# Optimization experiments

Hardware: AMD Instinct MI355X
Metric: run time of the kernel (lower is better)

The kernel has to match this reference:

```python
import jax, jax.numpy as jnp
import numpy as np

B, S, D_IN, D_MODEL = 128, 2048, 512, 2048
M, NSY, H, T = 25, 64, 8, 10
REP = NSY * (NSY + 1) // 2
OUT_DIMS = S * 2
DH = D_IN // H
IU, JU = np.triu_indices(NSY)
IDX_OUT = np.arange(NSY)                      # 'first-last': first n neurons for out sync
IDX_ACT = np.arange(D_MODEL - NSY, D_MODEL)   # last n neurons for action sync


def _ln(x, g, b):
    mu = x.mean(-1, keepdims=True)
    var = x.var(-1, keepdims=True)
    return (x - mu) / jnp.sqrt(var + 1e-5) * g + b


def _sync(act, alpha, beta, r, idx):
    # pairwise upper-triangle outer product without materializing (B,n,n)
    sel = act[:, idx]
    pair = sel[:, IU] * sel[:, JU]  # (B, REP)
    if alpha is None:
        alpha, beta = pair, jnp.ones_like(pair)
    else:
        alpha = r * alpha + pair
        beta = r * beta + 1.0
    return alpha / jnp.sqrt(beta), alpha, beta


def _forward(tokens, emb, W_pos, b_pos, Wq, bq, Wk, bk, Wv, bv, Wo, bo, Ws, bs,
             ln_s_g, ln_s_b, ln_n_g, ln_n_b, Wn, bn, temp, Wout, bout,
             start_act, start_trace, decay_action, decay_out):
    # rotary-style learned positional embedding: rotate [0,1] by theta in [0,180deg]
    thetas = jnp.deg2rad(jnp.linspace(0.0, 180.0, S))
    rotated = jnp.stack([-jnp.sin(thetas), jnp.cos(thetas)], -1)  # (S,2)
    pe = rotated @ W_pos + b_pos                                   # (S, D_IN)
    feats = emb[tokens] + pe[None]                                 # (B,S,D_IN)
    kh = (feats @ Wk + bk).reshape(B, S, H, DH)
    vh = (feats @ Wv + bv).reshape(B, S, H, DH)
    r_a = jnp.exp(-decay_action)[None]
    r_o = jnp.exp(-decay_out)[None]
    act = jnp.broadcast_to(start_act[None], (B, D_MODEL))
    trace = jnp.broadcast_to(start_trace[None], (B, D_MODEL, M))
    a_a = b_a = a_o = b_o = None
    preds, certs = [], []
    for _ in range(T):
        s_act, a_a, b_a = _sync(act, a_a, b_a, r_a, IDX_ACT)
        q = (s_act @ Wq + bq).reshape(B, H, DH)
        scores = jnp.einsum('bhd,bshd->bhs', q, kh) / np.float32(np.sqrt(DH))
        attn = jax.nn.softmax(scores, -1)
        o = jnp.einsum('bhs,bshd->bhd', attn, vh).reshape(B, D_IN) @ Wo + bo
        # SynapseNet: Linear -> GLU -> LayerNorm
        pre = jnp.concatenate([o, act], -1) @ Ws + bs
        g1, g2 = jnp.split(pre, 2, -1)
        state = _ln(g1 * jax.nn.sigmoid(g2), ln_s_g, ln_s_b)  # (B, D_MODEL)
        trace = jnp.concatenate([trace[:, :, 1:], state[:, :, None]], -1)
        # NLM: per-neuron linear over memory, GLU, temperature
        xn = _ln(trace, ln_n_g, ln_n_b)
        y = jnp.einsum('bnm,mon->bno', xn, Wn) + bn  # (B, D_MODEL, 2)
        act = (y[..., 0] * jax.nn.sigmoid(y[..., 1])) / temp
        s_out, a_o, b_o = _sync(act, a_o, b_o, r_o, IDX_OUT)
        pred = s_out @ Wout + bout  # (B, OUT_DIMS)
        preds.append(pred)
        logits = pred.reshape(B, S, 2)
        p = jax.nn.softmax(logits, -1)
        ent = -(p * jax.nn.log_softmax(logits, -1)).sum(-1) / np.float32(np.log(2.0))
        ne = ent.mean(-1)
        certs.append(jnp.stack([ne, 1.0 - ne], -1))
    return jnp.stack(preds, -1), jnp.stack(certs, -1)  # (B,OUT_DIMS,T),(B,2,T)


def setup_inputs() -> dict:
    key = jax.random.key(0)
    ks = jax.random.split(key, 16)
    def n(k, shape, s=0.02):
        return (jax.random.normal(k, shape) * s).astype(jnp.float32)
    bound = 1.0 / np.sqrt(M + 2)
    return {
        'tokens': jax.random.randint(ks[0], (B, S), 0, 2, dtype=jnp.int32),
        'emb': n(ks[1], (2, D_IN), 1.0),
        'W_pos': n(ks[2], (2, D_IN)), 'b_pos': jnp.zeros((D_IN,)),
        'Wq': n(ks[3], (REP, D_IN)), 'bq': jnp.zeros((D_IN,)),
        'Wk': n(ks[4], (D_IN, D_IN)), 'bk': jnp.zeros((D_IN,)),
        'Wv': n(ks[5], (D_IN, D_IN)), 'bv': jnp.zeros((D_IN,)),
        'Wo': n(ks[6], (D_IN, D_IN)), 'bo': jnp.zeros((D_IN,)),
        'Ws': n(ks[7], (D_IN + D_MODEL, 2 * D_MODEL)), 'bs': jnp.zeros((2 * D_MODEL,)),
        'ln_s_g': jnp.ones((D_MODEL,)), 'ln_s_b': jnp.zeros((D_MODEL,)),
        'ln_n_g': jnp.ones((M,)), 'ln_n_b': jnp.zeros((M,)),
        'Wn': jax.random.uniform(ks[8], (M, 2, D_MODEL), minval=-bound, maxval=bound),
        'bn': jnp.zeros((1, D_MODEL, 2)),
        'temp': jnp.ones((1,)),
        'Wout': n(ks[9], (REP, OUT_DIMS)), 'bout': jnp.zeros((OUT_DIMS,)),
        'start_act': n(ks[10], (D_MODEL,), 1.0),
        'start_trace': n(ks[11], (D_MODEL, M), 1.0),
        'decay_action': jax.random.uniform(ks[12], (REP,), minval=0.0, maxval=1.0),
        'decay_out': jax.random.uniform(ks[13], (REP,), minval=0.0, maxval=1.0),
    }


def reference(tokens, emb, W_pos, b_pos, Wq, bq, Wk, bk, Wv, bv, Wo, bo, Ws, bs,
              ln_s_g, ln_s_b, ln_n_g, ln_n_b, Wn, bn, temp, Wout, bout,
              start_act, start_trace, decay_action, decay_out):
    return _forward(tokens, emb, W_pos, b_pos, Wq, bq, Wk, bk, Wv, bv, Wo, bo, Ws, bs,
                    ln_s_g, ln_s_b, ln_n_g, ln_n_b, Wn, bn, temp, Wout, bout,
                    start_act, start_trace, decay_action, decay_out)
```

## Files before the change

### kernel.cpp

```cpp
#include <hip/hip_runtime.h>
#include <hip/hip_bf16.h>
#include <math.h>

#define B_ 128
#define S_ 2048
#define D_IN_ 512
#define D_MODEL_ 2048
#define M_ 25
#define NSY_ 64
#define H_ 8
#define T_ 10
#define REP_ 2080
#define DH_ 64
#define PRED_N (B_ * 4096)

typedef unsigned short ushort_t;
typedef __bf16 bf16x8 __attribute__((ext_vector_type(8)));
typedef float f32x4 __attribute__((ext_vector_type(4)));
typedef unsigned short us8 __attribute__((ext_vector_type(8)));

__device__ __forceinline__ ushort_t f2bf(float f) {
    __hip_bfloat16 h = __float2bfloat16(f);
    return *(ushort_t*)&h;
}

__global__ __launch_bounds__(256) void gemm_bf16(
    const float* __restrict__ A, int lda,
    const ushort_t* __restrict__ Bt, int ldb,
    const float* __restrict__ bias,
    float* __restrict__ C, int ldc,
    int M, int N, int K, int kchunk)
{
    const int nb = blockIdx.x, mb = blockIdx.y, zb = blockIdx.z;
    const int k0 = zb * kchunk;
    const int k1 = min(K, k0 + kchunk);
    __shared__ ushort_t As[64][40];
    __shared__ ushort_t Bs[128][40];

    const int tid  = threadIdx.x;
    const int wave = tid >> 6;
    const int lane = tid & 63;
    const int quad = lane >> 4;
    const int mrow = lane & 15;

    f32x4 acc[4][2];
    #pragma unroll
    for (int s = 0; s < 4; s++)
        #pragma unroll
        for (int u = 0; u < 2; u++)
            acc[s][u] = (f32x4){0.f, 0.f, 0.f, 0.f};

    const int arow = tid >> 2, akc = (tid & 3) * 8;
// ... 28 lines not shown
            for (int u = 0; u < 2; u++)
                acc[s][u] = __builtin_amdgcn_mfma_f32_16x16x32_bf16(
                    af[s], bfr[u], acc[s][u], 0, 0, 0);
        __syncthreads();
    }

    if (gridDim.z == 1) {
        #pragma unroll
        for (int s = 0; s < 4; s++)
            #pragma unroll
            for (int u = 0; u < 2; u++) {
                const int col = nb * 128 + wave * 32 + u * 16 + mrow;
                #pragma unroll
                for (int reg = 0; reg < 4; reg++) {
                    const int row = mb * 64 + s * 16 + quad * 4 + reg;
                    C[(size_t)row * ldc + col] = acc[s][u][reg] + bias[col];
                }
            }
    } else {
        #pragma unroll
        for (int s = 0; s < 4; s++)
            #pragma unroll
            for (int u = 0; u < 2; u++) {
                const int col = nb * 128 + wave * 32 + u * 16 + mrow;
                #pragma unroll
                for (int reg = 0; reg < 4; reg++) {
                    const int row = mb * 64 + s * 16 + quad * 4 + reg;
                    atomicAdd(&C[(size_t)row * ldc + col], acc[s][u][reg]);
                }
            }
    }
}

__global__ __launch_bounds__(256) void gemm_bb(
    const ushort_t* __restrict__ A, int lda,
    const ushort_t* __restrict__ Bt, int ldb,
    const float* __restrict__ bias,
    float* __restrict__ C, int ldc,
    int M, int N, int K, int kchunk)
{
    const int nb = blockIdx.x, mb = blockIdx.y, zb = blockIdx.z;
    const int k0 = zb * kchunk;
    const int k1 = min(K, k0 + kchunk);
    __shared__ ushort_t As[64][40];
    __shared__ ushort_t Bs[128][40];

    const int tid  = threadIdx.x;
    const int wave = tid >> 6;
    const int lane = tid & 63;
    const int quad = lane >> 4;
    const int mrow = lane & 15;

    f32x4 acc[4][2];
    #pragma unroll
    for (int s = 0; s < 4; s++)
        #pragma unroll
        for (int u = 0; u < 2; u++)
            acc[s][u] = (f32x4){0.f, 0.f, 0.f, 0.f};

    const int arow = tid >> 2, akc = (tid & 3) * 8;
    const int brow = tid >> 1, bkc = (tid & 1) * 16;

    for (int kk0 = k0; kk0 < k1; kk0 += 32) {
        {
            const ushort_t* ap = A + (size_t)(mb * 64 + arow) * lda + kk0 + akc;
            *(us8*)&As[arow][akc] = *(const us8*)ap;
        }
        {
            const ushort_t* bp = Bt + (size_t)(nb * 128 + brow) * ldb + kk0 + bkc;
            *(us8*)&Bs[brow][bkc]     = *(const us8*)bp;
            *(us8*)&Bs[brow][bkc + 8] = *(const us8*)(bp + 8);
        }
        __syncthreads();

        bf16x8 af[4], bfr[2];
        #pragma unroll
        for (int s = 0; s < 4; s++)
            af[s] = *(const bf16x8*)&As[s * 16 + mrow][quad * 8];
        #pragma unroll
        for (int u = 0; u < 2; u++)
            bfr[u] = *(const bf16x8*)&Bs[wave * 32 + u * 16 + mrow][quad * 8];
        #pragma unroll
        for (int s = 0; s < 4; s++)
            #pragma unroll
            for (int u = 0; u < 2; u++)
                acc[s][u] = __builtin_amdgcn_mfma_f32_16x16x32_bf16(
                    af[s], bfr[u], acc[s][u], 0, 0, 0);
        __syncthreads();
    }

    if (gridDim.z == 1) {
        #pragma unroll
        for (int s = 0; s < 4; s++)
            #pragma unroll
            for (int u = 0; u < 2; u++) {
                const int col = nb * 128 + wave * 32 + u * 16 + mrow;
                #pragma unroll
                for (int reg = 0; reg < 4; reg++) {
                    const int row = mb * 64 + s * 16 + quad * 4 + reg;
                    C[(size_t)row * ldc + col] = acc[s][u][reg] + bias[col];
                }
            }
    } else {
        #pragma unroll
        for (int s = 0; s < 4; s++)
            #pragma unroll
            for (int u = 0; u < 2; u++) {
                const int col = nb * 128 + wave * 32 + u * 16 + mrow;
                #pragma unroll
                for (int reg = 0; reg < 4; reg++) {
                    const int row = mb * 64 + s * 16 + quad * 4 + reg;
                    atomicAdd(&C[(size_t)row * ldc + col], acc[s][u][reg]);
                }
            }
    }
}

__device__ __forceinline__ void g_tile128(
    const ushort_t* Ap, int lda, const ushort_t* Bt, int ldb,
    float* C, int ldc, int nb, int mb, int k0, int k1, char* smem, int tid)
{
    ushort_t (*As)[40] = (ushort_t(*)[40])smem;
    ushort_t (*Bs)[40] = (ushort_t(*)[40])(smem + 64 * 40 * 2);
    const int wave = tid >> 6;
    const int lane = tid & 63;
    const int quad = lane >> 4;
    const int mrow = lane & 15;

    f32x4 acc[4][2];
    #pragma unroll
    for (int s = 0; s < 4; s++)
        #pragma unroll
        for (int u = 0; u < 2; u++)
            acc[s][u] = (f32x4){0.f, 0.f, 0.f, 0.f};

    const int arow = tid >> 2, akc = (tid & 3) * 8;
    const int brow = tid >> 1, bkc = (tid & 1) * 16;

    for (int kk0 = k0; kk0 < k1; kk0 += 32) {
        {
            const ushort_t* ap = Ap + (size_t)(mb * 64 + arow) * lda + kk0 + akc;
            *(us8*)&As[arow][akc] = *(const us8*)ap;
        }
        {
            const ushort_t* bp = Bt + (size_t)(nb * 128 + brow) * ldb + kk0 + bkc;
            *(us8*)&Bs[brow][bkc]     = *(const us8*)bp;
            *(us8*)&Bs[brow][bkc + 8] = *(const us8*)(bp + 8);
        }
// ... 28 lines not shown
        }
}

__global__ __launch_bounds__(256) void triple_kernel(
    const ushort_t* __restrict__ s_outb, const ushort_t* __restrict__ WoutT,
    float* __restrict__ predt,
    const ushort_t* __restrict__ s_actb, const ushort_t* __restrict__ WqT,
    float* __restrict__ qbuf,
    const ushort_t* __restrict__ actb, const ushort_t* __restrict__ WsT,
    float* __restrict__ pre_nxt)
{
    __shared__ __align__(16) char smem[15360];
    const int vb = blockIdx.x, tid = threadIdx.x;
    if (vb < 320) {
        const int nb = vb & 31, mb = (vb >> 5) & 1, zb = vb >> 6;
        const int k0 = zb * 416;
        g_tile128(s_outb, REP_, WoutT, REP_, predt, 4096,
                  nb, mb, k0, min(REP_, k0 + 416), smem, tid);
    } else if (vb < 424) {
        const int v2 = vb - 320;
        const int nb = v2 & 3, mb = (v2 >> 2) & 1, zb = v2 >> 3;
        const int k0 = zb * 160;
        g_tile128(s_actb, REP_, WqT, REP_, qbuf, 512,
                  nb, mb, k0, min(REP_, k0 + 160), smem, tid);
    } else {
        const int v3 = vb - 424;
        const int nb = v3 & 31, mb = (v3 >> 5) & 1, zb = v3 >> 6;
        const int k0 = zb * 256;
        g_tile128(actb, 2048, WsT + 512, 2560, pre_nxt, 4096,
                  nb, mb, k0, k0 + 256, smem, tid);
    }
}

__global__ __launch_bounds__(256) void gemm_qk(
    const float* __restrict__ q,
    const ushort_t* __restrict__ Kb,
    float* __restrict__ sc)
{
    const int nb = blockIdx.x, mb = blockIdx.y, z = blockIdx.z;
    const int c = z >> 3, h = z & 7;
    __shared__ ushort_t As[64][40];
    __shared__ ushort_t Bs[128][40];

    const int tid  = threadIdx.x;
    const int wave = tid >> 6;
    const int lane = tid & 63;
    const int quad = lane >> 4;
    const int mrow = lane & 15;

    f32x4 acc[4][2];
    #pragma unroll
    for (int s = 0; s < 4; s++)
        #pragma unroll
        for (int u = 0; u < 2; u++)
            acc[s][u] = (f32x4){0.f, 0.f, 0.f, 0.f};

    const int arow = tid >> 2, akc = (tid & 3) * 8;
    const int brow = tid >> 1, bkc = (tid & 1) * 16;
    const float* Abase = q + (size_t)h * 64;
    const ushort_t* Bbase = Kb + (size_t)c * S_ * 512 + h * 64;

    #pragma unroll
    for (int kk0 = 0; kk0 < 64; kk0 += 32) {
        {
            const float* ap = Abase + (size_t)(mb * 64 + arow) * 512 + kk0 + akc;
            float4 v0 = *(const float4*)ap;
            float4 v1 = *(const float4*)(ap + 4);
            us8 w = { f2bf(v0.x), f2bf(v0.y), f2bf(v0.z), f2bf(v0.w),
                      f2bf(v1.x), f2bf(v1.y), f2bf(v1.z), f2bf(v1.w) };
            *(us8*)&As[arow][akc] = w;
        }
        {
            const ushort_t* bp = Bbase + (size_t)(nb * 128 + brow) * 512 + kk0 + bkc;
            *(us8*)&Bs[brow][bkc]     = *(const us8*)bp;
            *(us8*)&Bs[brow][bkc + 8] = *(const us8*)(bp + 8);
        }
        __syncthreads();

        bf16x8 af[4], bfr[2];
        #pragma unroll
        for (int s = 0; s < 4; s++)
            af[s] = *(const bf16x8*)&As[s * 16 + mrow][quad * 8];
        #pragma unroll
        for (int u = 0; u < 2; u++)
            bfr[u] = *(const bf16x8*)&Bs[wave * 32 + u * 16 + mrow][quad * 8];
        #pragma unroll
        for (int s = 0; s < 4; s++)
            #pragma unroll
            for (int u = 0; u < 2; u++)
                acc[s][u] = __builtin_amdgcn_mfma_f32_16x16x32_bf16(
                    af[s], bfr[u], acc[s][u], 0, 0, 0);
        __syncthreads();
    }

    float* Cb = sc + (size_t)z * 128 * S_;
    #pragma unroll
    for (int s = 0; s < 4; s++)
        #pragma unroll
        for (int u = 0; u < 2; u++) {
            const int col = nb * 128 + wave * 32 + u * 16 + mrow;
            #pragma unroll
            for (int reg = 0; reg < 4; reg++) {
                const int row = mb * 64 + s * 16 + quad * 4 + reg;
                Cb[(size_t)row * S_ + col] = 0.125f * acc[s][u][reg];
            }
        }
}

__global__ __launch_bounds__(256) void attn_soft(
    const float* __restrict__ sc,
    const int*   __restrict__ tokens,
    ushort_t* __restrict__ P,
    float* __restrict__ o,
    const float* __restrict__ bs2,
    float* __restrict__ pre_nxt)
{
    const int bh = blockIdx.x;
    const int b = bh >> 3, h = bh & 7;
    __shared__ float red[256];
    const int tid = threadIdx.x;

    if (bh < 512) {
        const int idx = bh * 256 + tid;
        const float4* bs4 = (const float4*)bs2;
        ((float4*)pre_nxt)[idx] = bs4[idx & 1023];
    } else if (bh < 576) {
        const int idx = (bh - 512) * 256 + tid;
        ((float4*)o)[idx] = make_float4(0.f, 0.f, 0.f, 0.f);
    }

    const float* sc0 = sc + ((size_t)h * 128 + b) * S_;
    const float* sc1 = sc + ((size_t)(8 + h) * 128 + b) * S_;
    const int* trow = tokens + (size_t)b * S_;

    int tok[8]; float sel[8];
    float lmax = -1e30f;
    #pragma unroll
    for (int i = 0; i < 8; i++) {
        const int s = tid + i * 256;
        tok[i] = trow[s];
        sel[i] = tok[i] ? sc1[s] : sc0[s];
        lmax = fmaxf(lmax, sel[i]);
    }
    red[tid] = lmax; __syncthreads();
    for (int off = 128; off > 0; off >>= 1) {
        if (tid < off) red[tid] = fmaxf(red[tid], red[tid + off]);
        __syncthreads();
    }
    const float mx = red[0];
    __syncthreads();

    float e[8];
    float lsum = 0.f;
    #pragma unroll
    for (int i = 0; i < 8; i++) {
        e[i] = expf(sel[i] - mx);
        lsum += e[i];
    }
    red[tid] = lsum; __syncthreads();
    for (int off = 128; off > 0; off >>= 1) {
        if (tid < off) red[tid] += red[tid + off];
        __syncthreads();
    }
    const float inv = 1.f / red[0];

    ushort_t* Pb = P + ((size_t)h * 128 + b) * 4096;
    #pragma unroll
    for (int i = 0; i < 8; i++) {
        const int s = tid + i * 256;
        const unsigned p = (unsigned)f2bf(e[i] * inv);
        const unsigned word = tok[i] ? (p << 16) : p;
        *(unsigned*)&Pb[s * 2] = word;
    }
}

__global__ __launch_bounds__(256) void gemm_pv(
    const ushort_t* __restrict__ P,
    const ushort_t* __restrict__ VT,
    float* __restrict__ o)
{
    const int mb = blockIdx.x, h = blockIdx.y, zb = blockIdx.z;
    const int k0 = zb * 512;
    __shared__ ushort_t As[64][40];
    __shared__ ushort_t Bs[64][40];

    const int tid  = threadIdx.x;
    const int wave = tid >> 6;
    const int lane = tid & 63;
    const int quad = lane >> 4;
    const int mrow = lane & 15;

    f32x4 acc[4];
    #pragma unroll
    for (int s = 0; s < 4; s++) acc[s] = (f32x4){0.f, 0.f, 0.f, 0.f};

    const int row = tid >> 2, kc = (tid & 3) * 8;
    const ushort_t* Ab = P  + ((size_t)h * 128 + mb * 64 + row) * 4096;
    const ushort_t* Bb = VT + ((size_t)h * 64 + row) * 4096;

    for (int kk = k0; kk < k0 + 512; kk += 32) {
        *(us8*)&As[row][kc] = *(const us8*)(Ab + kk + kc);
        *(us8*)&Bs[row][kc] = *(const us8*)(Bb + kk + kc);
        __syncthreads();
        bf16x8 bfr = *(const bf16x8*)&Bs[wave * 16 + mrow][quad * 8];
        #pragma unroll
        for (int s = 0; s < 4; s++) {
            bf16x8 af = *(const bf16x8*)&As[s * 16 + mrow][quad * 8];
            acc[s] = __builtin_amdgcn_mfma_f32_16x16x32_bf16(af, bfr, acc[s], 0, 0, 0);
        }
        __syncthreads();
    }

    const int col = h * 64 + wave * 16 + mrow;
    #pragma unroll
    for (int s = 0; s < 4; s++)
        #pragma unroll
        for (int reg = 0; reg < 4; reg++) {
            const int rowi = mb * 64 + s * 16 + quad * 4 + reg;
            atomicAdd(&o[(size_t)rowi * 512 + col], acc[s][reg]);
        }
}

__global__ void build_vt(const float* __restrict__ Vtab, ushort_t* __restrict__ VT)
{
    const int gid = blockIdx.x * 256 + threadIdx.x;
    const int k = gid & 4095;
    const int d = (gid >> 12) & 63;
    const int h = gid >> 18;
    const int s = k >> 1, c = k & 1;
    VT[gid] = f2bf(Vtab[((size_t)(c * S_ + s)) * 512 + h * 64 + d]);
}

#define IA_FE 8192
#define IA_AC (IA_FE + 1024)
#define IA_TR (IA_AC + 6400)
#define IA_SY (IA_TR + 9)
#define IA_NB (IA_SY + 1)
__global__ void init_all(const float* __restrict__ emb, const float* __restrict__ Wp,
                         const float* __restrict__ bp, float* __restrict__ f2,
                         const float* __restrict__ sa, float* __restrict__ act,
                         ushort_t* __restrict__ actb,
                         const float* __restrict__ st, float* __restrict__ trace,
                         const float* __restrict__ dec_act, const float* __restrict__ dec_out,
                         int* __restrict__ ijtab, float* __restrict__ r_act,
                         float* __restrict__ r_out, float* __restrict__ sqb_a,
                         float* __restrict__ sqb_o, float* __restrict__ zerov)
{
    const int vb = blockIdx.x, tid = threadIdx.x;
    if (vb < IA_FE) {
        const int gid = vb * 256 + tid;
        const int k = gid & 511;
        const int s = (gid >> 9) & (S_ - 1);
        const int c = gid >> 20;
        const float th = 3.14159265358979323846f * (float)s / (float)(S_ - 1);
        f2[gid] = emb[c * 512 + k] + (-sinf(th)) * Wp[k] + cosf(th) * Wp[512 + k] + bp[k];
    } else if (vb < IA_AC) {
        const int gid = (vb - IA_FE) * 256 + tid;
        const int n = gid & 2047;
        const float v = sa[n];
        act[gid] = v;
        actb[gid] = f2bf(v);
    } else if (vb < IA_TR) {
        const int idx4 = (vb - IA_AC) * 256 + tid;
        ((float4*)trace)[idx4] = ((const float4*)st)[idx4 % 12800];
    } else if (vb < IA_SY) {
        const int p = (vb - IA_TR) * 256 + tid;
        if (p >= REP_) return;
        int i = 0, rem = p;
        while (rem >= NSY_ - i) { rem -= NSY_ - i; i++; }
        ijtab[p] = (i << 16) | (i + rem);
        const float ra = expf(-dec_act[p]);
        const float ro = expf(-dec_out[p]);
        r_act[p] = ra; r_out[p] = ro;
        float ba = 1.f, bo2 = 1.f;
        sqb_a[p] = 1.f;
        sqb_o[p] = 1.f;
        for (int t = 1; t < T_; t++) {
            ba  = ra * ba  + 1.f;
            bo2 = ro * bo2 + 1.f;
            sqb_a[(size_t)t * REP_ + p] = sqrtf(ba);
            sqb_o[(size_t)t * REP_ + p] = sqrtf(bo2);
        }
    } else {
        #pragma unroll
        for (int k = 0; k < 4; k++)
            ((float4*)zerov)[tid * 4 + k] = make_float4(0.f, 0.f, 0.f, 0.f);
    }
}

__global__ __launch_bounds__(256) void transpose_all(
    const float* __restrict__ Wk, ushort_t* __restrict__ WkT,
    const float* __restrict__ Wv, ushort_t* __restrict__ WvT,
    const float* __restrict__ Wq, ushort_t* __restrict__ WqT,
    const float* __restrict__ Wo, ushort_t* __restrict__ WoT,
    const float* __restrict__ Ws, ushort_t* __restrict__ WsT,
    const float* __restrict__ Wout, ushort_t* __restrict__ WoutT)
{
    int bid = blockIdx.x;
    const float* in; ushort_t* out; int K, N;
    if      (bid <   256) {              in = Wk;   out = WkT;   K = 512;  N = 512;  }
    else if (bid <   512) { bid -=  256; in = Wv;   out = WvT;   K = 512;  N = 512;  }
    else if (bid <  1552) { bid -=  512; in = Wq;   out = WqT;   K = 2080; N = 512;  }
    else if (bid <  1808) { bid -= 1552; in = Wo;   out = WoT;   K = 512;  N = 512;  }
    else if (bid < 12048) { bid -= 1808; in = Ws;   out = WsT;   K = 2560; N = 4096; }
    else                  { bid -= 12048; in = Wout; out = WoutT; K = 2080; N = 4096; }
    const int bxw = N >> 5;
    const int bx = bid % bxw, by = bid / bxw;
    __shared__ float tile[32][33];
    const int k0 = by * 32, n0 = bx * 32;
    const int tx = threadIdx.x & 31, ty4 = (threadIdx.x >> 5) * 4;
    #pragma unroll
    for (int i = 0; i < 4; i++)
        tile[ty4 + i][tx] = in[(size_t)(k0 + ty4 + i) * N + n0 + tx];
    __syncthreads();
    #pragma unroll
    for (int i = 0; i < 4; i++)
        out[(size_t)(n0 + ty4 + i) * K + k0 + tx] = f2bf(tile[tx][ty4 + i]);
}

__global__ void cast_bf16_kernel(const float* __restrict__ src,
                                 __hip_bfloat16* __restrict__ dst, int n)
{
    const int gid = (blockIdx.x * 256 + threadIdx.x) * 4;
    if (gid >= n) return;
    float4 v = *(const float4*)(src + gid);
    dst[gid + 0] = __float2bfloat16(v.x);
    dst[gid + 1] = __float2bfloat16(v.y);
    dst[gid + 2] = __float2bfloat16(v.z);
    dst[gid + 3] = __float2bfloat16(v.w);
}

__global__ void bs2_kernel(const float* __restrict__ bs, const float* __restrict__ bo,
                           const float* __restrict__ Ws, float* __restrict__ bs2)
{
    const int n = blockIdx.x * 256 + threadIdx.x;
    float acc = bs[n];
    for (int j = 0; j < 512; j++)
        acc += bo[j] * Ws[(size_t)j * 4096 + n];
    bs2[n] = acc;
}

__global__ void sync_kernel(const float* __restrict__ act,
                            float* __restrict__ alpha,
                            const float* __restrict__ decay,
                            const int t, const int off,
                            ushort_t* __restrict__ sout,
                            float* __restrict__ ib1, const float* __restrict__ bias1, int iN1,
                            float* __restrict__ ib2, const float* __restrict__ bias2, int iN2)
{
    const int b = blockIdx.x;
    const int tid = threadIdx.x;
    if (blockIdx.y == 8) {
        if (ib1)
            for (int n = tid; n < iN1; n += 256)
                ib1[(size_t)b * iN1 + n] = bias1[n];
        if (ib2)
            for (int n = tid; n < iN2; n += 256)
                ib2[(size_t)b * iN2 + n] = bias2[n];
    }
    const int p = blockIdx.y * 256 + tid;
    if (p >= REP_) return;
    int i = 0, rem = p;
    while (rem >= NSY_ - i) { rem -= NSY_ - i; i++; }
    const int j = i + rem;
    const float si = act[(size_t)b * D_MODEL_ + off + i];
    const float sj = act[(size_t)b * D_MODEL_ + off + j];
    const float pair = si * sj;
    const float r = expf(-decay[p]);
    float a;
    if (t == 0) a = pair;
    else        a = r * alpha[(size_t)b * REP_ + p] + pair;
    alpha[(size_t)b * REP_ + p] = a;
// ... 89 lines not shown
        }
    }
    __syncthreads();

    if (half == 0) {
        for (int p = tid; p < REP_; p += 512) {
            const int ij = ijtab[p];
            const float pair = sh_sync[ij >> 16] * sh_sync[ij & 0xffff];
            const float r = r_out[p];
            float a2;
            if (TT == 0) a2 = pair;
            else         a2 = r * a_o[(size_t)b * REP_ + p] + pair;
            a_o[(size_t)b * REP_ + p] = a2;
            s_outb[(size_t)b * REP_ + p] = f2bf(a2 / sqb_out[(size_t)TT * REP_ + p]);
        }
        const float4* b4 = (const float4*)bout;
        float4* pd = (float4*)(predt + (size_t)b * 4096);
        for (int idx = tid; idx < 1024; idx += 512) pd[idx] = b4[idx];
    } else if (TT < T_ - 1) {
        for (int p = tid; p < REP_; p += 512) {
            const int ij = ijtab[p];
            const float pair = sh_sync[ij >> 16] * sh_sync[ij & 0xffff];
            const float r = r_act[p];
            float a2 = r * a_a[(size_t)b * REP_ + p] + pair;
            a_a[(size_t)b * REP_ + p] = a2;
            s_actb[(size_t)b * REP_ + p] = f2bf(a2 / sqb_act[(size_t)(TT + 1) * REP_ + p]);
        }
        const float4* b4 = (const float4*)bq;
        float4* qb = (float4*)(qbuf + (size_t)b * 512);
        if (tid < 128) qb[tid] = b4[tid];
    }
}

__global__ __launch_bounds__(256) void ent_all_kernel(
    const float* __restrict__ predst,
    float* __restrict__ certbf)
{
    const int t = blockIdx.x >> 7;
    const int b = blockIdx.x & 127;
    const int tid = threadIdx.x;
    __shared__ float red[256];
    const float* pr = predst + (size_t)t * PRED_N + (size_t)b * 4096;
    float sum = 0.f;
    #pragma unroll
    for (int i = 0; i < 8; i++) {
        const int s = tid + i * 256;
        const float l0 = pr[2 * s], l1 = pr[2 * s + 1];
        const float mm = fmaxf(l0, l1);
        const float z0 = expf(l0 - mm), z1 = expf(l1 - mm);
        const float Z = z0 + z1;
        const float lz = logf(Z);
        const float p0 = z0 / Z, p1 = z1 / Z;
        const float lp0 = (l0 - mm) - lz, lp1 = (l1 - mm) - lz;
        sum += -(p0 * lp0 + p1 * lp1) * 1.4426950408889634f;
    }
    red[tid] = sum; __syncthreads();
    for (int off = 128; off > 0; off >>= 1) {
        if (tid < off) red[tid] += red[tid + off];
        __syncthreads();
    }
    if (tid == 0) {
        const float ne = red[0] * (1.f / S_);
        certbf[(size_t)t * B_ * 2 + b * 2 + 0] = ne;
        certbf[(size_t)t * B_ * 2 + b * 2 + 1] = 1.f - ne;
    }
}

__global__ __launch_bounds__(256) void finalize_kernel(
    const float* __restrict__ predstage,
    const float* __restrict__ certbuf,
    float* __restrict__ dout)
{
    __shared__ float tile[T_][1024];
    const int tid = threadIdx.x;
    const int row0 = blockIdx.x * 1024;
    #pragma unroll
    for (int t = 0; t < T_; t++) {
        float4 v = *(const float4*)(predstage + (size_t)t * PRED_N + row0 + tid * 4);
        tile[t][tid * 4 + 0] = v.x; tile[t][tid * 4 + 1] = v.y;
        tile[t][tid * 4 + 2] = v.z; tile[t][tid * 4 + 3] = v.w;
    }
    __syncthreads();
    float buf[40];
    #pragma unroll
    for (int r = 0; r < 4; r++)
        #pragma unroll
        for (int t = 0; t < T_; t++)
            buf[r * 10 + t] = tile[t][tid * 4 + r];
    float* dst = dout + (size_t)(row0 + tid * 4) * T_;
    #pragma unroll
    for (int k = 0; k < 10; k++)
        *(float4*)(dst + k * 4) = make_float4(buf[4*k], buf[4*k+1], buf[4*k+2], buf[4*k+3]);

    if (blockIdx.x == 0 && tid < B_) {
        const int b = tid;
        const size_t base = (size_t)PRED_N * T_;
        #pragma unroll
        for (int t = 0; t < T_; t++) {
            dout[base + (size_t)(b * 2 + 0) * T_ + t] = certbuf[t * B_ * 2 + b * 2 + 0];
            dout[base + (size_t)(b * 2 + 1) * T_ + t] = certbuf[t * B_ * 2 + b * 2 + 1];
        }
    }
}

extern "C" void kernel_launch(void* const* d_in, const int* in_sizes, int n_in,
                              void* d_out, int out_size, void* d_ws, size_t ws_size,
                              hipStream_t stream)
{
    const int*   tokens    = (const int*)  d_in[0];
    const float* emb       = (const float*)d_in[1];
    const float* W_pos     = (const float*)d_in[2];
    const float* b_pos     = (const float*)d_in[3];
    const float* Wq        = (const float*)d_in[4];
    const float* bq        = (const float*)d_in[5];
    const float* Wk        = (const float*)d_in[6];
    const float* bk        = (const float*)d_in[7];
    const float* Wv        = (const float*)d_in[8];
    const float* bv        = (const float*)d_in[9];
    const float* Wo        = (const float*)d_in[10];
    const float* bo        = (const float*)d_in[11];
    const float* Ws        = (const float*)d_in[12];
    const float* bs        = (const float*)d_in[13];
    const float* ln_s_g    = (const float*)d_in[14];
    const float* ln_s_b    = (const float*)d_in[15];
    const float* ln_n_g    = (const float*)d_in[16];
    const float* ln_n_b    = (const float*)d_in[17];
    const float* Wn        = (const float*)d_in[18];
    const float* bn        = (const float*)d_in[19];
    const float* temp      = (const float*)d_in[20];
    const float* Wout      = (const float*)d_in[21];
    const float* bout      = (const float*)d_in[22];
    const float* start_act = (const float*)d_in[23];
    const float* start_tr  = (const float*)d_in[24];
    const float* dec_act   = (const float*)d_in[25];
    const float* dec_out   = (const float*)d_in[26];
    float* out = (float*)d_out;
    float* w = (float*)d_ws;

    size_t off = 0;
    float* f2     = w + off; off += (size_t)2 * S_ * 512;
    float* Ktab   = w + off; off += (size_t)2 * S_ * 512;
    float* Vtab   = w + off; off += (size_t)2 * S_ * 512;
    float* act    = w + off; off += (size_t)B_ * D_MODEL_;
    float* a_a    = w + off; off += (size_t)B_ * REP_;
    float* a_o    = w + off; off += (size_t)B_ * REP_;
    float* qbuf   = w + off; off += (size_t)B_ * 512;
    float* o_attn = w + off; off += (size_t)B_ * 512;
    float* pre0   = w + off; off += (size_t)B_ * 4096;
    float* pre1   = w + off; off += (size_t)B_ * 4096;
    float* trace  = w + off; off += (size_t)B_ * D_MODEL_ * M_;
    float* scbuf  = w + off; off += (size_t)16 * 128 * S_;
    float* predst = w + off; off += (size_t)T_ * PRED_N;
    float* certbf = w + off; off += (size_t)T_ * B_ * 2;
    float* Wcomb32= w + off; off += (size_t)4096 * 512;
    float* bs2    = w + off; off += 4096;
    float* zerov  = w + off; off += 4096;
    ushort_t* s_actb = (ushort_t*)(w + off); off += (size_t)B_ * REP_ / 2;
    ushort_t* s_outb = (ushort_t*)(w + off); off += (size_t)B_ * REP_ / 2;
    ushort_t* actb   = (ushort_t*)(w + off); off += (size_t)B_ * D_MODEL_ / 2;
    __hip_bfloat16* Kb = (__hip_bfloat16*)(w + off); off += (size_t)S_ * 512;
    ushort_t* Pbuf  = (ushort_t*)(w + off); off += (size_t)8 * 128 * 4096 / 2;
    ushort_t* VT    = (ushort_t*)(w + off); off += (size_t)8 * 64 * 4096 / 2;
    ushort_t* WkT   = (ushort_t*)(w + off); off += (size_t)512 * 512 / 2;
    ushort_t* WvT   = (ushort_t*)(w + off); off += (size_t)512 * 512 / 2;
    ushort_t* WqT   = (ushort_t*)(w + off); off += (size_t)512 * REP_ / 2;
    ushort_t* WoT   = (ushort_t*)(w + off); off += (size_t)512 * 512 / 2;
    ushort_t* WsT   = (ushort_t*)(w + off); off += (size_t)4096 * 2560 / 2;
    ushort_t* WoutT = (ushort_t*)(w + off); off += (size_t)4096 * REP_ / 2;
    ushort_t* WoC   = (ushort_t*)(w + off); off += (size_t)512 * 512 / 2;
    ushort_t* WcombTb=(ushort_t*)(w + off); off += (size_t)4096 * 512 / 2;
    int*   ijtab  = (int*)(w + off); off += REP_;
    float* r_actT = w + off; off += REP_;
    float* r_outT = w + off; off += REP_;
    float* sqb_a  = w + off; off += (size_t)T_ * REP_;
    float* sqb_o  = w + off; off += (size_t)T_ * REP_;

    init_all<<<IA_NB, 256, 0, stream>>>(
        emb, W_pos, b_pos, f2, start_act, act, actb, start_tr, trace,
        dec_act, dec_out, ijtab, r_actT, r_outT, sqb_a, sqb_o, zerov);
    transpose_all<<<20368, 256, 0, stream>>>(
        Wk, WkT, Wv, WvT, Wq, WqT, Wo, WoT, Ws, WsT, Wout, WoutT);
    gemm_bf16<<<dim3(4, 64, 1), 256, 0, stream>>>(
        f2, 512, WkT, 512, bk, Ktab, 512, 2 * S_, 512, 512, 512);
    gemm_bf16<<<dim3(4, 64, 1), 256, 0, stream>>>(
        f2, 512, WvT, 512, bv, Vtab, 512, 2 * S_, 512, 512, 512);
    cast_bf16_kernel<<<(2 * S_ * 512 / 4) / 256, 256, 0, stream>>>(Ktab, Kb, 2 * S_ * 512);
    build_vt<<<(8 * 64 * 4096) / 256, 256, 0, stream>>>(Vtab, VT);

    cast_bf16_kernel<<<(512 * 512 / 4) / 256, 256, 0, stream>>>(
        Wo, (__hip_bfloat16*)WoC, 512 * 512);
    gemm_bb<<<dim3(4, 64, 1), 256, 0, stream>>>(
        WsT, 2560, WoC, 512, zerov, Wcomb32, 512, 4096, 512, 512, 512);
    cast_bf16_kernel<<<(4096 * 512 / 4) / 256, 256, 0, stream>>>(
        Wcomb32, (__hip_bfloat16*)WcombTb, 4096 * 512);
    bs2_kernel<<<16, 256, 0, stream>>>(bs, bo, Ws, bs2);

    sync_kernel<<<dim3(B_, 9), 256, 0, stream>>>(
        act, a_a, dec_act, 0, D_MODEL_ - NSY_, s_actb,
        qbuf, bq, 512, pre0, bs2, 4096);
    gemm_bb<<<dim3(32, 2, 8), 256, 0, stream>>>(
        actb, 2048, WsT + 512, 2560, zerov, pre0, 4096, B_, 4096, 2048, 256);
    gemm_bb<<<dim3(4, 2, 13), 256, 0, stream>>>(
        s_actb, REP_, WqT, REP_, zerov, qbuf, 512, B_, 512, REP_, 160);

    #define ST_ARGS(PC, PT) \
        PC, ln_s_g, ln_s_b, trace, ln_n_g, ln_n_b, Wn, bn, temp, actb, \
        ijtab, r_outT, sqb_o, a_o, s_outb, bout, PT, \
        r_actT, sqb_a, a_a, s_actb, bq, qbuf

    for (int t = 0; t < T_; t++) {
        float* pre_cur = (t & 1) ? pre1 : pre0;
        float* pre_nxt = (t & 1) ? pre0 : pre1;
        float* predt = predst + (size_t)t * PRED_N;

        gemm_qk<<<dim3(S_ / 128, 2, 16), 256, 0, stream>>>(
            qbuf, (const ushort_t*)Kb, scbuf);
        attn_soft<<<B_ * H_, 256, 0, stream>>>(
            scbuf, tokens, Pbuf, o_attn, bs2, pre_nxt);
        gemm_pv<<<dim3(2, 8, 8), 256, 0, stream>>>(Pbuf, VT, o_attn);

        gemm_bf16<<<dim3(32, 2, 4), 256, 0, stream>>>(
            o_attn, 512, WcombTb, 512, bs2, pre_cur, 4096, B_, 4096, 512, 128);

        switch (t) {
            case 0: st_kernel<0><<<B_ * 2, 512, 0, stream>>>(ST_ARGS(pre_cur, predt)); break;
            case 1: st_kernel<1><<<B_ * 2, 512, 0, stream>>>(ST_ARGS(pre_cur, predt)); break;
            case 2: st_kernel<2><<<B_ * 2, 512, 0, stream>>>(ST_ARGS(pre_cur, predt)); break;
            case 3: st_kernel<3><<<B_ * 2, 512, 0, stream>>>(ST_ARGS(pre_cur, predt)); break;
            case 4: st_kernel<4><<<B_ * 2, 512, 0, stream>>>(ST_ARGS(pre_cur, predt)); break;
            case 5: st_kernel<5><<<B_ * 2, 512, 0, stream>>>(ST_ARGS(pre_cur, predt)); break;
            case 6: st_kernel<6><<<B_ * 2, 512, 0, stream>>>(ST_ARGS(pre_cur, predt)); break;
            case 7: st_kernel<7><<<B_ * 2, 512, 0, stream>>>(ST_ARGS(pre_cur, predt)); break;
            case 8: st_kernel<8><<<B_ * 2, 512, 0, stream>>>(ST_ARGS(pre_cur, predt)); break;
            case 9: st_kernel<9><<<B_ * 2, 512, 0, stream>>>(ST_ARGS(pre_cur, predt)); break;
        }

        const int nblk = (t < T_ - 1) ? 936 : 320;
        triple_kernel<<<nblk, 256, 0, stream>>>(
            s_outb, WoutT, predt, s_actb, WqT, qbuf, actb, WsT, pre_nxt);
    }

    ent_all_kernel<<<T_ * B_, 256, 0, stream>>>(predst, certbf);
    finalize_kernel<<<PRED_N / 1024, 256, 0, stream>>>(predst, certbf, out);
}
```

Measured before the change: 1.157 ms.

## Fuse setup kernels, select QK scores by token bitmask, merge epilogue kernels

Several setup launches are merged into a few multi-role kernels. The K/V projection GEMMs and the Wcomb GEMM become one grid, and the bf16 casts plus the V transpose become another. The initial Ws and Wq GEMMs are merged, and the Wo cast, bias fold and a token bitmask move into init_all. The QK kernel now writes only the score that matches each token's choice into a half-size buffer, which cuts score writes and the softmax read. The PV GEMM is split across more k-chunks, and the entropy and finalize kernels are fused into one per-batch epilogue. This trades fewer launches and less traffic for more divergent multi-role kernels and an epilogue grid of only 128 blocks.

```diff
diff --git a/kernel.cpp b/kernel.cpp
--- a/kernel.cpp
+++ b/kernel.cpp
@@ -18,6 +18,7 @@
 typedef __bf16 bf16x8 __attribute__((ext_vector_type(8)));
 typedef float f32x4 __attribute__((ext_vector_type(4)));
 typedef unsigned short us8 __attribute__((ext_vector_type(8)));
+typedef unsigned short us4 __attribute__((ext_vector_type(4)));
 
 __device__ __forceinline__ ushort_t f2bf(float f) {
     __hip_bfloat16 h = __float2bfloat16(f);
@@ -112,16 +113,18 @@
     }
 }
 
-__global__ __launch_bounds__(256) void gemm_bb(
-    const ushort_t* __restrict__ A, int lda,
-    const ushort_t* __restrict__ Bt, int ldb,
-    const float* __restrict__ bias,
-    float* __restrict__ C, int ldc,
-    int M, int N, int K, int kchunk)
-{
-    const int nb = blockIdx.x, mb = blockIdx.y, zb = blockIdx.z;
-    const int k0 = zb * kchunk;
-    const int k1 = min(K, k0 + kchunk);
+__global__ __launch_bounds__(256) void gemm3_kernel(
+    const float* __restrict__ f2,
+    const ushort_t* __restrict__ WkT, const float* __restrict__ bk, float* __restrict__ Ktab,
+    const ushort_t* __restrict__ WvT, const float* __restrict__ bv, float* __restrict__ Vtab,
+    const ushort_t* __restrict__ WsT, const ushort_t* __restrict__ WoC,
+    const float* __restrict__ zerov, float* __restrict__ Wcomb32)
+{
+    const int nb = blockIdx.x, mb = blockIdx.y, zs = blockIdx.z;
+    const ushort_t* Bt = (zs == 0) ? WkT : (zs == 1) ? WvT : WoC;
+    const float* bias  = (zs == 0) ? bk  : (zs == 1) ? bv  : zerov;
+    float* C           = (zs == 0) ? Ktab : (zs == 1) ? Vtab : Wcomb32;
+
     __shared__ ushort_t As[64][40];
     __shared__ ushort_t Bs[128][40];
 
@@ -141,13 +144,20 @@
     const int arow = tid >> 2, akc = (tid & 3) * 8;
     const int brow = tid >> 1, bkc = (tid & 1) * 16;
 
-    for (int kk0 = k0; kk0 < k1; kk0 += 32) {
+    for (int kk0 = 0; kk0 < 512; kk0 += 32) {
+        if (zs < 2) {
+            const float* ap = f2 + (size_t)(mb * 64 + arow) * 512 + kk0 + akc;
+            float4 v0 = *(const float4*)ap;
+            float4 v1 = *(const float4*)(ap + 4);
+            us8 w = { f2bf(v0.x), f2bf(v0.y), f2bf(v0.z), f2bf(v0.w),
+                      f2bf(v1.x), f2bf(v1.y), f2bf(v1.z), f2bf(v1.w) };
+            *(us8*)&As[arow][akc] = w;
+        } else {
+            const ushort_t* ap = WsT + (size_t)(mb * 64 + arow) * 2560 + kk0 + akc;
+            *(us8*)&As[arow][akc] = *(const us8*)ap;
+        }
         {
-            const ushort_t* ap = A + (size_t)(mb * 64 + arow) * lda + kk0 + akc;
-            *(us8*)&As[arow][akc] = *(const us8*)ap;
-        }
-        {
-            const ushort_t* bp = Bt + (size_t)(nb * 128 + brow) * ldb + kk0 + bkc;
+            const ushort_t* bp = Bt + (size_t)(nb * 128 + brow) * 512 + kk0 + bkc;
             *(us8*)&Bs[brow][bkc]     = *(const us8*)bp;
             *(us8*)&Bs[brow][bkc + 8] = *(const us8*)(bp + 8);
         }
@@ -169,31 +179,17 @@
         __syncthreads();
     }
 
-    if (gridDim.z == 1) {
-        #pragma unroll
-        for (int s = 0; s < 4; s++)
+    #pragma unroll
+    for (int s = 0; s < 4; s++)
+        #pragma unroll
+        for (int u = 0; u < 2; u++) {
+            const int col = nb * 128 + wave * 32 + u * 16 + mrow;
             #pragma unroll
-            for (int u = 0; u < 2; u++) {
-                const int col = nb * 128 + wave * 32 + u * 16 + mrow;
-                #pragma unroll
-                for (int reg = 0; reg < 4; reg++) {
-                    const int row = mb * 64 + s * 16 + quad * 4 + reg;
-                    C[(size_t)row * ldc + col] = acc[s][u][reg] + bias[col];
-                }
+            for (int reg = 0; reg < 4; reg++) {
+                const int row = mb * 64 + s * 16 + quad * 4 + reg;
+                C[(size_t)row * 512 + col] = acc[s][u][reg] + bias[col];
             }
-    } else {
-        #pragma unroll
-        for (int s = 0; s < 4; s++)
-            #pragma unroll
-            for (int u = 0; u < 2; u++) {
-                const int col = nb * 128 + wave * 32 + u * 16 + mrow;
-                #pragma unroll
-                for (int reg = 0; reg < 4; reg++) {
-                    const int row = mb * 64 + s * 16 + quad * 4 + reg;
-                    atomicAdd(&C[(size_t)row * ldc + col], acc[s][u][reg]);
-                }
-            }
-    }
+        }
 }
 
 __device__ __forceinline__ void g_tile128(
@@ -288,10 +284,33 @@
     }
 }
 
-__global__ __launch_bounds__(256) void gemm_qk(
+__global__ __launch_bounds__(256) void dual0_kernel(
+    const ushort_t* __restrict__ actb, const ushort_t* __restrict__ WsT,
+    float* __restrict__ pre0,
+    const ushort_t* __restrict__ s_actb, const ushort_t* __restrict__ WqT,
+    float* __restrict__ qbuf)
+{
+    __shared__ __align__(16) char smem[15360];
+    const int vb = blockIdx.x, tid = threadIdx.x;
+    if (vb < 512) {
+        const int nb = vb & 31, mb = (vb >> 5) & 1, zb = vb >> 6;
+        const int k0 = zb * 256;
+        g_tile128(actb, 2048, WsT + 512, 2560, pre0, 4096,
+                  nb, mb, k0, k0 + 256, smem, tid);
+    } else {
+        const int v2 = vb - 512;
+        const int nb = v2 & 3, mb = (v2 >> 2) & 1, zb = v2 >> 3;
+        const int k0 = zb * 160;
+        g_tile128(s_actb, REP_, WqT, REP_, qbuf, 512,
+                  nb, mb, k0, min(REP_, k0 + 160), smem, tid);
+    }
+}
+
+__global__ __launch_bounds__(256) void gemm_qk_sel(
     const float* __restrict__ q,
     const ushort_t* __restrict__ Kb,
-    float* __restrict__ sc)
+    const unsigned* __restrict__ tokbit,
+    float* __restrict__ scsel)
 {
     const int nb = blockIdx.x, mb = blockIdx.y, z = blockIdx.z;
     const int c = z >> 3, h = z & 7;
@@ -349,22 +368,34 @@
         __syncthreads();
     }
 
-    float* Cb = sc + (size_t)z * 128 * S_;
+    const int colw = nb * 4 + wave;
+    unsigned tb[16];
+    #pragma unroll
+    for (int s = 0; s < 4; s++)
+        #pragma unroll
+        for (int reg = 0; reg < 4; reg++) {
+            const int row = mb * 64 + s * 16 + quad * 4 + reg;
+            tb[s * 4 + reg] = tokbit[row * 64 + colw];
+        }
+
+    float* Cb = scsel + (size_t)h * 128 * S_;
     #pragma unroll
     for (int s = 0; s < 4; s++)
         #pragma unroll
         for (int u = 0; u < 2; u++) {
             const int col = nb * 128 + wave * 32 + u * 16 + mrow;
+            const int sh = (u * 16 + mrow) & 31;
             #pragma unroll
             for (int reg = 0; reg < 4; reg++) {
                 const int row = mb * 64 + s * 16 + quad * 4 + reg;
-                Cb[(size_t)row * S_ + col] = 0.125f * acc[s][u][reg];
+                if (((tb[s * 4 + reg] >> sh) & 1u) == (unsigned)c)
+                    Cb[(size_t)row * S_ + col] = 0.125f * acc[s][u][reg];
             }
         }
 }
 
 __global__ __launch_bounds__(256) void attn_soft(
-    const float* __restrict__ sc,
+    const float* __restrict__ scsel,
     const int*   __restrict__ tokens,
     ushort_t* __restrict__ P,
     float* __restrict__ o,
@@ -385,8 +416,7 @@
         ((float4*)o)[idx] = make_float4(0.f, 0.f, 0.f, 0.f);
     }
 
-    const float* sc0 = sc + ((size_t)h * 128 + b) * S_;
-    const float* sc1 = sc + ((size_t)(8 + h) * 128 + b) * S_;
+    const float* scs = scsel + ((size_t)h * 128 + b) * S_;
     const int* trow = tokens + (size_t)b * S_;
 
     int tok[8]; float sel[8];
@@ -395,7 +425,7 @@
     for (int i = 0; i < 8; i++) {
         const int s = tid + i * 256;
         tok[i] = trow[s];
-        sel[i] = tok[i] ? sc1[s] : sc0[s];
+        sel[i] = scs[s];
         lmax = fmaxf(lmax, sel[i]);
     }
     red[tid] = lmax; __syncthreads();
@@ -436,7 +466,7 @@
     float* __restrict__ o)
 {
     const int mb = blockIdx.x, h = blockIdx.y, zb = blockIdx.z;
-    const int k0 = zb * 512;
+    const int k0 = zb * 256;
     __shared__ ushort_t As[64][40];
     __shared__ ushort_t Bs[64][40];
 
@@ -454,7 +484,7 @@
     const ushort_t* Ab = P  + ((size_t)h * 128 + mb * 64 + row) * 4096;
     const ushort_t* Bb = VT + ((size_t)h * 64 + row) * 4096;
 
-    for (int kk = k0; kk < k0 + 512; kk += 32) {
+    for (int kk = k0; kk < k0 + 256; kk += 32) {
         *(us8*)&As[row][kc] = *(const us8*)(Ab + kk + kc);
         *(us8*)&Bs[row][kc] = *(const us8*)(Bb + kk + kc);
         __syncthreads();
@@ -475,23 +505,16 @@
             const int rowi = mb * 64 + s * 16 + quad * 4 + reg;
             atomicAdd(&o[(size_t)rowi * 512 + col], acc[s][reg]);
         }
-}
-
-__global__ void build_vt(const float* __restrict__ Vtab, ushort_t* __restrict__ VT)
-{
-    const int gid = blockIdx.x * 256 + threadIdx.x;
-    const int k = gid & 4095;
-    const int d = (gid >> 12) & 63;
-    const int h = gid >> 18;
-    const int s = k >> 1, c = k & 1;
-    VT[gid] = f2bf(Vtab[((size_t)(c * S_ + s)) * 512 + h * 64 + d]);
 }
 
 #define IA_FE 8192
 #define IA_AC (IA_FE + 1024)
 #define IA_TR (IA_AC + 6400)
 #define IA_SY (IA_TR + 9)
-#define IA_NB (IA_SY + 1)
+#define IA_ZV (IA_SY + 1)
+#define IA_WO (IA_ZV + 256)
+#define IA_BS (IA_WO + 16)
+#define IA_NB (IA_BS + 1024)
 __global__ void init_all(const float* __restrict__ emb, const float* __restrict__ Wp,
                          const float* __restrict__ bp, float* __restrict__ f2,
                          const float* __restrict__ sa, float* __restrict__ act,
@@ -500,7 +523,11 @@
                          const float* __restrict__ dec_act, const float* __restrict__ dec_out,
                          int* __restrict__ ijtab, float* __restrict__ r_act,
                          float* __restrict__ r_out, float* __restrict__ sqb_a,
-                         float* __restrict__ sqb_o, float* __restrict__ zerov)
+                         float* __restrict__ sqb_o, float* __restrict__ zerov,
+                         const float* __restrict__ Wo, ushort_t* __restrict__ WoC,
+                         const float* __restrict__ bs, const float* __restrict__ bo,
+                         const float* __restrict__ Ws, float* __restrict__ bs2,
+                         const int* __restrict__ tokens, unsigned* __restrict__ tokbit)
 {
     const int vb = blockIdx.x, tid = threadIdx.x;
     if (vb < IA_FE) {
@@ -537,10 +564,31 @@
             sqb_a[(size_t)t * REP_ + p] = sqrtf(ba);
             sqb_o[(size_t)t * REP_ + p] = sqrtf(bo2);
         }
-    } else {
+    } else if (vb < IA_ZV) {
         #pragma unroll
         for (int k = 0; k < 4; k++)
             ((float4*)zerov)[tid * 4 + k] = make_float4(0.f, 0.f, 0.f, 0.f);
+    } else if (vb < IA_WO) {
+        const int idx4 = (vb - IA_ZV) * 256 + tid;
+        float4 v = ((const float4*)Wo)[idx4];
+        us4 w = { f2bf(v.x), f2bf(v.y), f2bf(v.z), f2bf(v.w) };
+        ((us4*)WoC)[idx4] = w;
+    } else if (vb < IA_BS) {
+        const int n = (vb - IA_WO) * 256 + tid;
+        float acc = bs[n];
+        for (int j = 0; j < 512; j++)
+            acc += bo[j] * Ws[(size_t)j * 4096 + n];
+        bs2[n] = acc;
+    } else {
+        const int blk = vb - IA_BS;
+        const int b = blk >> 3, s0 = (blk & 7) * 256;
+        const int tok = tokens[(size_t)b * S_ + s0 + tid];
+        const unsigned long long m = __ballot(tok != 0);
+        if ((tid & 63) == 0) {
+            const int w = tid >> 6;
+            tokbit[b * 64 + (s0 >> 5) + w * 2]     = (unsigned)m;
+            tokbit[b * 64 + (s0 >> 5) + w * 2 + 1] = (unsigned)(m >> 32);
+        }
     }
 }
 
@@ -574,26 +622,29 @@
         out[(size_t)(n0 + ty4 + i) * K + k0 + tx] = f2bf(tile[tx][ty4 + i]);
 }
 
-__global__ void cast_bf16_kernel(const float* __restrict__ src,
-                                 __hip_bfloat16* __restrict__ dst, int n)
-{
-    const int gid = (blockIdx.x * 256 + threadIdx.x) * 4;
-    if (gid >= n) return;
-    float4 v = *(const float4*)(src + gid);
-    dst[gid + 0] = __float2bfloat16(v.x);
-    dst[gid + 1] = __float2bfloat16(v.y);
-    dst[gid + 2] = __float2bfloat16(v.z);
-    dst[gid + 3] = __float2bfloat16(v.w);
-}
-
-__global__ void bs2_kernel(const float* __restrict__ bs, const float* __restrict__ bo,
-                           const float* __restrict__ Ws, float* __restrict__ bs2)
-{
-    const int n = blockIdx.x * 256 + threadIdx.x;
-    float acc = bs[n];
-    for (int j = 0; j < 512; j++)
-        acc += bo[j] * Ws[(size_t)j * 4096 + n];
-    bs2[n] = acc;
+__global__ void cast3_kernel(const float* __restrict__ Ktab, ushort_t* __restrict__ Kb,
+                             const float* __restrict__ Vtab, ushort_t* __restrict__ VT,
+                             const float* __restrict__ Wcomb32, ushort_t* __restrict__ WcombTb)
+{
+    const int vb = blockIdx.x, tid = threadIdx.x;
+    if (vb < 2048) {
+        const int idx4 = vb * 256 + tid;
+        float4 v = ((const float4*)Ktab)[idx4];
+        us4 w = { f2bf(v.x), f2bf(v.y), f2bf(v.z), f2bf(v.w) };
+        ((us4*)Kb)[idx4] = w;
+    } else if (vb < 10240) {
+        const int gid = (vb - 2048) * 256 + tid;
+        const int k = gid & 4095;
+        const int d = (gid >> 12) & 63;
+        const int h = gid >> 18;
+        const int s = k >> 1, c = k & 1;
+        VT[gid] = f2bf(Vtab[((size_t)(c * S_ + s)) * 512 + h * 64 + d]);
+    } else {
+        const int idx4 = (vb - 10240) * 256 + tid;
+        float4 v = ((const float4*)Wcomb32)[idx4];
+        us4 w = { f2bf(v.x), f2bf(v.y), f2bf(v.z), f2bf(v.w) };
+        ((us4*)WcombTb)[idx4] = w;
+    }
 }
 
 __global__ void sync_kernel(const float* __restrict__ act,
@@ -749,75 +800,74 @@
     }
 }
 
-__global__ __launch_bounds__(256) void ent_all_kernel(
+__global__ __launch_bounds__(256) void epilogue_kernel(
     const float* __restrict__ predst,
-    float* __restrict__ certbf)
-{
-    const int t = blockIdx.x >> 7;
-    const int b = blockIdx.x & 127;
-    const int tid = threadIdx.x;
+    float* __restrict__ dout)
+{
+    __shared__ float tile[T_][1024];
     __shared__ float red[256];
-    const float* pr = predst + (size_t)t * PRED_N + (size_t)b * 4096;
-    float sum = 0.f;
-    #pragma unroll
-    for (int i = 0; i < 8; i++) {
-        const int s = tid + i * 256;
-        const float l0 = pr[2 * s], l1 = pr[2 * s + 1];
-        const float mm = fmaxf(l0, l1);
-        const float z0 = expf(l0 - mm), z1 = expf(l1 - mm);
-        const float Z = z0 + z1;
-        const float lz = logf(Z);
-        const float p0 = z0 / Z, p1 = z1 / Z;
-        const float lp0 = (l0 - mm) - lz, lp1 = (l1 - mm) - lz;
-        sum += -(p0 * lp0 + p1 * lp1) * 1.4426950408889634f;
-    }
-    red[tid] = sum; __syncthreads();
-    for (int off = 128; off > 0; off >>= 1) {
-        if (tid < off) red[tid] += red[tid + off];
-        __syncthreads();
-    }
-    if (tid == 0) {
-        const float ne = red[0] * (1.f / S_);
-        certbf[(size_t)t * B_ * 2 + b * 2 + 0] = ne;
-        certbf[(size_t)t * B_ * 2 + b * 2 + 1] = 1.f - ne;
-    }
-}
-
-__global__ __launch_bounds__(256) void finalize_kernel(
-    const float* __restrict__ predstage,
-    const float* __restrict__ certbuf,
-    float* __restrict__ dout)
-{
-    __shared__ float tile[T_][1024];
-    const int tid = threadIdx.x;
-    const int row0 = blockIdx.x * 1024;
+    __shared__ float certv[T_];
+    const int b = blockIdx.x, tid = threadIdx.x;
+
+    float esum[T_];
+    #pragma unroll
+    for (int t = 0; t < T_; t++) esum[t] = 0.f;
+
+    for (int c4 = 0; c4 < 4; c4++) {
+        const int row0 = c4 * 1024;
+        #pragma unroll
+        for (int t = 0; t < T_; t++) {
+            float4 v = *(const float4*)(predst + (size_t)t * PRED_N
+                                        + (size_t)b * 4096 + row0 + tid * 4);
+            tile[t][tid * 4 + 0] = v.x; tile[t][tid * 4 + 1] = v.y;
+            tile[t][tid * 4 + 2] = v.z; tile[t][tid * 4 + 3] = v.w;
+            {
+                const float mm = fmaxf(v.x, v.y);
+                const float z0 = expf(v.x - mm), z1 = expf(v.y - mm);
+                const float Z = z0 + z1, lz = logf(Z);
+                const float p0 = z0 / Z, p1 = z1 / Z;
+                esum[t] += -(p0 * ((v.x - mm) - lz) + p1 * ((v.y - mm) - lz))
+                           * 1.4426950408889634f;
+            }
+            {
+                const float mm = fmaxf(v.z, v.w);
+                const float z0 = expf(v.z - mm), z1 = expf(v.w - mm);
+                const float Z = z0 + z1, lz = logf(Z);
+                const float p0 = z0 / Z, p1 = z1 / Z;
+                esum[t] += -(p0 * ((v.z - mm) - lz) + p1 * ((v.w - mm) - lz))
+                           * 1.4426950408889634f;
+            }
+        }
+        __syncthreads();
+        float buf[40];
+        #pragma unroll
+        for (int r = 0; r < 4; r++)
+            #pragma unroll
+            for (int t = 0; t < T_; t++)
+                buf[r * 10 + t] = tile[t][tid * 4 + r];
+        float* dst = dout + ((size_t)b * 4096 + row0 + tid * 4) * T_;
+        #pragma unroll
+        for (int k = 0; k < 10; k++)
+            *(float4*)(dst + k * 4) = make_float4(buf[4*k], buf[4*k+1], buf[4*k+2], buf[4*k+3]);
+        __syncthreads();
+    }
+
     #pragma unroll
     for (int t = 0; t < T_; t++) {
-        float4 v = *(const float4*)(predstage + (size_t)t * PRED_N + row0 + tid * 4);
-        tile[t][tid * 4 + 0] = v.x; tile[t][tid * 4 + 1] = v.y;
-        tile[t][tid * 4 + 2] = v.z; tile[t][tid * 4 + 3] = v.w;
-    }
-    __syncthreads();
-    float buf[40];
-    #pragma unroll
-    for (int r = 0; r < 4; r++)
-        #pragma unroll
-        for (int t = 0; t < T_; t++)
-            buf[r * 10 + t] = tile[t][tid * 4 + r];
-    float* dst = dout + (size_t)(row0 + tid * 4) * T_;
-    #pragma unroll
-    for (int k = 0; k < 10; k++)
-        *(float4*)(dst + k * 4) = make_float4(buf[4*k], buf[4*k+1], buf[4*k+2], buf[4*k+3]);
-
-    if (blockIdx.x == 0 && tid < B_) {
-        const int b = tid;
-        const size_t base = (size_t)PRED_N * T_;
-        #pragma unroll
-        for (int t = 0; t < T_; t++) {
-            dout[base + (size_t)(b * 2 + 0) * T_ + t] = certbuf[t * B_ * 2 + b * 2 + 0];
-            dout[base + (size_t)(b * 2 + 1) * T_ + t] = certbuf[t * B_ * 2 + b * 2 + 1];
-        }
-    }
+        red[tid] = esum[t]; __syncthreads();
+        for (int off = 128; off > 0; off >>= 1) {
+            if (tid < off) red[tid] += red[tid + off];
+            __syncthreads();
+        }
+        if (tid == 0) certv[t] = red[0] * (1.f / S_);
+        __syncthreads();
+    }
+
+    const size_t base = (size_t)PRED_N * T_;
+    if (tid < T_)
+        dout[base + (size_t)(b * 2 + 0) * T_ + tid] = certv[tid];
+    else if (tid < 2 * T_)
+        dout[base + (size_t)(b * 2 + 1) * T_ + (tid - T_)] = 1.f - certv[tid - T_];
 }
 
 extern "C" void kernel_launch(void* const* d_in, const int* in_sizes, int n_in,
@@ -866,9 +916,8 @@
     float* pre0   = w + off; off += (size_t)B_ * 4096;
     float* pre1   = w + off; off += (size_t)B_ * 4096;
     float* trace  = w + off; off += (size_t)B_ * D_MODEL_ * M_;
-    float* scbuf  = w + off; off += (size_t)16 * 128 * S_;
+    float* scsel  = w + off; off += (size_t)8 * 128 * S_;
     float* predst = w + off; off += (size_t)T_ * PRED_N;
-    float* certbf = w + off; off += (size_t)T_ * B_ * 2;
     float* Wcomb32= w + off; off += (size_t)4096 * 512;
     float* bs2    = w + off; off += 4096;
     float* zerov  = w + off; off += 4096;
@@ -891,34 +940,22 @@
     float* r_outT = w + off; off += REP_;
     float* sqb_a  = w + off; off += (size_t)T_ * REP_;
     float* sqb_o  = w + off; off += (size_t)T_ * REP_;
+    unsigned* tokbit = (unsigned*)(w + off); off += (size_t)B_ * 64 / 1;
 
     init_all<<<IA_NB, 256, 0, stream>>>(
         emb, W_pos, b_pos, f2, start_act, act, actb, start_tr, trace,
-        dec_act, dec_out, ijtab, r_actT, r_outT, sqb_a, sqb_o, zerov);
+        dec_act, dec_out, ijtab, r_actT, r_outT, sqb_a, sqb_o, zerov,
+        Wo, WoC, bs, bo, Ws, bs2, tokens, tokbit);
     transpose_all<<<20368, 256, 0, stream>>>(
         Wk, WkT, Wv, WvT, Wq, WqT, Wo, WoT, Ws, WsT, Wout, WoutT);
-    gemm_bf16<<<dim3(4, 64, 1), 256, 0, stream>>>(
-        f2, 512, WkT, 512, bk, Ktab, 512, 2 * S_, 512, 512, 512);
-    gemm_bf16<<<dim3(4, 64, 1), 256, 0, stream>>>(
-        f2, 512, WvT, 512, bv, Vtab, 512, 2 * S_, 512, 512, 512);
-    cast_bf16_kernel<<<(2 * S_ * 512 / 4) / 256, 256, 0, stream>>>(Ktab, Kb, 2 * S_ * 512);
-    build_vt<<<(8 * 64 * 4096) / 256, 256, 0, stream>>>(Vtab, VT);
-
-    cast_bf16_kernel<<<(512 * 512 / 4) / 256, 256, 0, stream>>>(
-        Wo, (__hip_bfloat16*)WoC, 512 * 512);
-    gemm_bb<<<dim3(4, 64, 1), 256, 0, stream>>>(
-        WsT, 2560, WoC, 512, zerov, Wcomb32, 512, 4096, 512, 512, 512);
-    cast_bf16_kernel<<<(4096 * 512 / 4) / 256, 256, 0, stream>>>(
-        Wcomb32, (__hip_bfloat16*)WcombTb, 4096 * 512);
-    bs2_kernel<<<16, 256, 0, stream>>>(bs, bo, Ws, bs2);
-
+    gemm3_kernel<<<dim3(4, 64, 3), 256, 0, stream>>>(
+        f2, WkT, bk, Ktab, WvT, bv, Vtab, WsT, WoC, zerov, Wcomb32);
+    cast3_kernel<<<12288, 256, 0, stream>>>(
+        Ktab, (ushort_t*)Kb, Vtab, VT, Wcomb32, WcombTb);
     sync_kernel<<<dim3(B_, 9), 256, 0, stream>>>(
         act, a_a, dec_act, 0, D_MODEL_ - NSY_, s_actb,
         qbuf, bq, 512, pre0, bs2, 4096);
-    gemm_bb<<<dim3(32, 2, 8), 256, 0, stream>>>(
-        actb, 2048, WsT + 512, 2560, zerov, pre0, 4096, B_, 4096, 2048, 256);
-    gemm_bb<<<dim3(4, 2, 13), 256, 0, stream>>>(
-        s_actb, REP_, WqT, REP_, zerov, qbuf, 512, B_, 512, REP_, 160);
+    dual0_kernel<<<616, 256, 0, stream>>>(actb, WsT, pre0, s_actb, WqT, qbuf);
 
     #define ST_ARGS(PC, PT) \
         PC, ln_s_g, ln_s_b, trace, ln_n_g, ln_n_b, Wn, bn, temp, actb, \
@@ -930,11 +967,11 @@
         float* pre_nxt = (t & 1) ? pre0 : pre1;
         float* predt = predst + (size_t)t * PRED_N;
 
-        gemm_qk<<<dim3(S_ / 128, 2, 16), 256, 0, stream>>>(
-            qbuf, (const ushort_t*)Kb, scbuf);
+        gemm_qk_sel<<<dim3(S_ / 128, 2, 16), 256, 0, stream>>>(
+            qbuf, (const ushort_t*)Kb, tokbit, scsel);
         attn_soft<<<B_ * H_, 256, 0, stream>>>(
-            scbuf, tokens, Pbuf, o_attn, bs2, pre_nxt);
-        gemm_pv<<<dim3(2, 8, 8), 256, 0, stream>>>(Pbuf, VT, o_attn);
+            scsel, tokens, Pbuf, o_attn, bs2, pre_nxt);
+        gemm_pv<<<dim3(2, 8, 16), 256, 0, stream>>>(Pbuf, VT, o_attn);
 
         gemm_bf16<<<dim3(32, 2, 4), 256, 0, stream>>>(
             o_attn, 512, WcombTb, 512, bs2, pre_cur, 4096, B_, 4096, 512, 128);
@@ -957,6 +994,5 @@
             s_outb, WoutT, predt, s_actb, WqT, qbuf, actb, WsT, pre_nxt);
     }
 
-    ent_all_kernel<<<T_ * B_, 256, 0, stream>>>(predst, certbf);
-    finalize_kernel<<<PRED_N / 1024, 256, 0, stream>>>(predst, certbf, out);
-}
+    epilogue_kernel<<<B_, 256, 0, stream>>>(predst, out);
+}
```

Result: faster. 1.113 ms (-3.8%).
